# Kernel tuning notes

Measured on AMD Instinct MI355X. Metric: run time of the kernel, lower is better.

## Reference

```python
import jax, jax.numpy as jnp
import numpy as np

B, S, E, G = 64, 24, 128, 256
Km, Kch, Ko, Kp, Kc = 100, 200, 50, 50, 30
Vm, Vch, Vo, Vp, Vl, Vc = 1000, 3000, 500, 1500, 700, 2000
Veth, Vgen, Vage, Vins = 10, 2, 100, 5
TOTK = Km + Kch + Ko + Kp + 1 + Kc + 4  # 435 concat width


def setup_inputs() -> dict:
    key = jax.random.key(0)
    ks = jax.random.split(key, 24)
    ri = lambda k, shape, hi: jax.random.randint(k, shape, 0, hi)
    rn = lambda k, shape: (jax.random.normal(k, shape, dtype=jnp.float32) * 0.02)
    return {
        'meds': ri(ks[0], (B, S, Km), Vm),
        'chart': ri(ks[1], (B, S, Kch), Vch),
        'out': ri(ks[2], (B, S, Ko), Vo),
        'proc': ri(ks[3], (B, S, Kp), Vp),
        'lab': ri(ks[4], (B, S), Vl),
        'conds': ri(ks[5], (B, Kc), Vc),
        'demo': ri(ks[6], (B, 4), 2),
        'med_E': rn(ks[7], (Vm, E)), 'chart_E': rn(ks[8], (Vch, E)),
        'out_E': rn(ks[9], (Vo, E)), 'proc_E': rn(ks[10], (Vp, E)),
        'lab_E': rn(ks[11], (Vl, E)), 'cond_E': rn(ks[12], (Vc, E)),
        'gender_E': rn(ks[13], (Vgen, E)), 'eth_E': rn(ks[14], (Veth, E)),
        'ins_E': rn(ks[15], (Vins, E)), 'age_E': rn(ks[16], (Vage, E)),
        'proj_W': rn(ks[17], (TOTK, E)), 'proj_b': jnp.zeros((E,), jnp.float32),
        'W1': rn(ks[18], (E, G)), 'b1': jnp.zeros((G,), jnp.float32),
        'W2': rn(ks[19], (G, G)), 'b2': jnp.zeros((G,), jnp.float32),
        'fc1_W': rn(ks[20], (G, G // 2)), 'fc1_b': jnp.zeros((G // 2,), jnp.float32),
        'fc2_W': rn(ks[21], (G // 2, 1)), 'fc2_b': jnp.zeros((1,), jnp.float32),
    }


def _forward(meds, chart, out, proc, lab, conds, demo,
             med_E, chart_E, out_E, proc_E, lab_E, cond_E,
             gender_E, eth_E, ins_E, age_E,
             proj_W, proj_b, W1, b1, W2, b2, fc1_W, fc1_b, fc2_W, fc2_b):
    clamp = lambda i, V: jnp.clip(i, 0, V - 1)
    med_e = med_E[clamp(meds, Vm)]        # [B,S,Km,E]
    chart_e = chart_E[clamp(chart, Vch)]  # [B,S,Kch,E]
    out_e = out_E[clamp(out, Vo)]         # [B,S,Ko,E]
    proc_e = proc_E[clamp(proc, Vp)]      # [B,S,Kp,E]
    lab_e = lab_E[clamp(lab, Vl)]         # [B,S,E]
    cond_e = cond_E[clamp(conds, Vc)]     # [B,Kc,E]
    gen_e = gender_E[demo[:, 0]]          # [B,E]
    eth_e = eth_E[demo[:, 1]]
    ins_e = ins_E[demo[:, 2]]
    age_e = age_E[demo[:, 3]]
    demo_cols = [jnp.broadcast_to(d[:, None, :, None], (B, S, E, 1))
                 for d in (gen_e, eth_e, ins_e, age_e)]
    x = jnp.concatenate([
        med_e.transpose(0, 1, 3, 2),    # [B,S,E,Km]
        chart_e.transpose(0, 1, 3, 2),
        out_e.transpose(0, 1, 3, 2),
        proc_e.transpose(0, 1, 3, 2),
        lab_e[..., None],               # [B,S,E,1]
        jnp.broadcast_to(cond_e[:, None], (B, S, Kc, E)).transpose(0, 1, 3, 2),
    ] + demo_cols, axis=-1)             # [B,S,E,TOTK]
    x = x.mean(axis=-2)                 # mean over embed dim -> [B,S,TOTK]
    N = B * S
    x = x.reshape(N, TOTK) @ proj_W + proj_b   # [N,E]
    # GCNConv over complete graph + self loops: normalized adjacency is 1/N
    # everywhere, so aggregation == node-mean of (x @ W).
    h = jnp.broadcast_to(jnp.mean(x @ W1, axis=0, keepdims=True) + b1, (N, G))
    h = jax.nn.relu(h)
    # entropy attention
    w = jnp.exp(-jnp.sum(h * jnp.log(h + 1e-9), axis=1))
    h = h * (w / jnp.sum(w))[:, None]
    h = jnp.broadcast_to(jnp.mean(h @ W2, axis=0, keepdims=True) + b2, (N, G))
    x_pooled = h.reshape(B, S, G).mean(axis=1)          # [B,G]
    f = jax.nn.relu(x_pooled @ fc1_W + fc1_b)           # [B,G/2]
    o = f @ fc2_W + fc2_b                               # [B,1]
    return jax.nn.sigmoid(o), o


def reference(meds, chart, out, proc, lab, conds, demo,
              med_E, chart_E, out_E, proc_E, lab_E, cond_E,
              gender_E, eth_E, ins_E, age_E,
              proj_W, proj_b, W1, b1, W2, b2, fc1_W, fc1_b, fc2_W, fc2_b):
    return _forward(meds, chart, out, proc, lab, conds, demo,
                    med_E, chart_E, out_E, proc_E, lab_E, cond_E,
                    gender_E, eth_E, ins_E, age_E,
                    proj_W, proj_b, W1, b1, W2, b2, fc1_W, fc1_b, fc2_W, fc2_b)
```

## Files before the change

### kernel.cpp

```cpp
#include <hip/hip_runtime.h>
#include <math.h>

#define B_ 64
#define S_ 24
#define E_ 128
#define G_ 256
#define N_ (B_ * S_)
#define Km_ 100
#define Kch_ 200
#define Ko_ 50
#define Kp_ 50
#define Kc_ 30
#define TOTK_ 435

#define Vm_ 1000
#define Vch_ 3000
#define Vo_ 500
#define Vp_ 1500
#define Vl_ 700
#define Vc_ 2000
#define TOTROWS_ 8817

#define OFF_MED 0
#define OFF_CHART 1000
#define OFF_OUT 4000
#define OFF_PROC 4500
#define OFF_LAB 6000
#define OFF_COND 6700
#define OFF_GEN 8700
#define OFF_ETH 8702
#define OFF_INS 8712
#define OFF_AGE 8717
#define OFF_PART 8832

#define NCHUNK_ 32
#define CHUNK_N_ 48
#define NBLK_B_ 129
#define NTHR_ 512

__device__ __forceinline__ int clampi(int v, int hi) {
    return v < 0 ? 0 : (v > hi ? hi : v);
}

__global__ __launch_bounds__(NTHR_) void rowmeans_kernel(
    const float* __restrict__ medE, const float* __restrict__ chartE,
    const float* __restrict__ outE, const float* __restrict__ procE,
    const float* __restrict__ labE, const float* __restrict__ condE,
    const float* __restrict__ genE, const float* __restrict__ ethE,
    const float* __restrict__ insE, const float* __restrict__ ageE,
    float* __restrict__ rm)
{
    int row = blockIdx.x * (NTHR_ / 64) + (threadIdx.x >> 6);
    int lane = threadIdx.x & 63;
    if (row >= TOTROWS_) return;

    const float* src;
    int r = row;
    if (r < Vm_)                  { src = medE; }
    else if ((r -= Vm_)  < Vch_)  { src = chartE; }
    else if ((r -= Vch_) < Vo_)   { src = outE; }
    else if ((r -= Vo_)  < Vp_)   { src = procE; }
    else if ((r -= Vp_)  < Vl_)   { src = labE; }
    else if ((r -= Vl_)  < Vc_)   { src = condE; }
    else if ((r -= Vc_)  < 2)     { src = genE; }
    else if ((r -= 2)    < 10)    { src = ethE; }
    else if ((r -= 10)   < 5)     { src = insE; }
    else                          { r -= 5; src = ageE; }

    float2 v = *reinterpret_cast<const float2*>(src + (size_t)r * E_ + lane * 2);
    float s = v.x + v.y;
    #pragma unroll
    for (int off = 32; off > 0; off >>= 1) s += __shfl_down(s, off, 64);
    if (lane == 0) rm[row] = s * (1.0f / E_);
}

template<int K, int RPI, int CBASE, int RMBASE, int VMAX>
__device__ __forceinline__ void table_chunk(
    const int* __restrict__ idx, const float* __restrict__ rm,
    float* __restrict__ part, int p, int t, float* __restrict__ lds)
{
    constexpr int ACT = K * RPI;
    float acc = 0.0f;
    if (t < ACT) {
        const int kk = t % K;
        const int nr = t / K;
        const int n0 = p * CHUNK_N_;
        #pragma unroll
        for (int i = 0; i < (CHUNK_N_ + RPI - 1) / RPI; ++i) {
            int n = n0 + nr + i * RPI;
            if (nr + i * RPI < CHUNK_N_) {
                int ix = clampi(idx[n * K + kk], VMAX);
                acc += rm[RMBASE + ix];
            }
        }
    }
    lds[t] = acc;
    __syncthreads();
    if (t < K) {
        float s = lds[t];
        #pragma unroll
        for (int r = 1; r < RPI; ++r) s += lds[r * K + t];
        part[(CBASE + t) * NCHUNK_ + p] = s;
    }
}

__global__ __launch_bounds__(NTHR_) void colsum_kernel(
    const int* __restrict__ meds, const int* __restrict__ chart,
    const int* __restrict__ outv, const int* __restrict__ proc,
    const int* __restrict__ lab,  const int* __restrict__ conds,
    const int* __restrict__ demo,
    const float* __restrict__ rm, float* __restrict__ part)
{
    __shared__ float lds_red[NTHR_];
    const int t = threadIdx.x;
    const int bid = blockIdx.x;

    if (bid < 128) {
        const int table = bid >> 5;
        const int p = bid & 31;
        if (table == 0)      table_chunk<Km_, 5, 0,   OFF_MED,  Vm_ -1>(meds,  rm, part, p, t, lds_red);
        else if (table == 1) table_chunk<Kch_,2, 100, OFF_CHART,Vch_-1>(chart, rm, part, p, t, lds_red);
        else if (table == 2) table_chunk<Ko_, 10,300, OFF_OUT,  Vo_ -1>(outv,  rm, part, p, t, lds_red);
        else                 table_chunk<Kp_, 10,350, OFF_PROC, Vp_ -1>(proc,  rm, part, p, t, lds_red);
    } else {
        const int lane = t & 63;
        const int w = t >> 6;
        for (int j = w; j < 35; j += 8) {
            float s = 0.0f;
            if (j == 0) {
                #pragma unroll
                for (int i = 0; i < 24; ++i)
                    s += rm[OFF_LAB + clampi(lab[lane + 64 * i], Vl_ - 1)];
            } else if (j < 31) {
                int kk = j - 1;
                s = rm[OFF_COND + clampi(conds[lane * Kc_ + kk], Vc_ - 1)];
            } else {
                int jj = j - 31;
                int base = (jj == 0) ? OFF_GEN : (jj == 1) ? OFF_ETH :
                           (jj == 2) ? OFF_INS : OFF_AGE;
                s = rm[base + demo[lane * 4 + jj]];
            }
            #pragma unroll
            for (int off = 32; off > 0; off >>= 1) s += __shfl_down(s, off, 64);
            if (lane == 0) part[(400 + j) * NCHUNK_] = s;
        }
    }
}

__global__ __launch_bounds__(NTHR_) void head_kernel(
    const float* __restrict__ part,
    const float* __restrict__ projW, const float* __restrict__ projb,
    const float* __restrict__ W1, const float* __restrict__ b1,
    const float* __restrict__ W2, const float* __restrict__ b2,
    const float* __restrict__ fc1W, const float* __restrict__ fc1b,
    const float* __restrict__ fc2W, const float* __restrict__ fc2b,
    float* __restrict__ outp)
{
    __shared__ float sm[TOTK_];
    __shared__ float xbar[E_];
    __shared__ float h1s[G_];
    __shared__ float h2s[G_];
    __shared__ float fsh[G_ / 2];
    __shared__ float4 part4[8][64];
    __shared__ float2 part2[8][64];
    __shared__ float hred[8];
    __shared__ float oval;

    const int t = threadIdx.x;
    const int lane = t & 63;
    const int oc = t >> 6;

    if (t < TOTK_) {
        const float4* pp = (const float4*)(part + t * NCHUNK_);
        float s;
        if (t < 400) {
            s = 0.f;
            #pragma unroll
            for (int j = 0; j < NCHUNK_ / 4; ++j) {
                float4 v = pp[j];
                s += (v.x + v.y) + (v.z + v.w);
            }
            s *= (1.0f / N_);
        } else if (t == 400) {
            s = part[t * NCHUNK_] * (1.0f / N_);
        } else {
            s = part[t * NCHUNK_] * (1.0f / B_);
        }
        sm[t] = s;
    }
    __syncthreads();

    {
        const float2* Wp = (const float2*)projW;
        const int k0 = (TOTK_ * oc) >> 3;
        const int k1 = (TOTK_ * (oc + 1)) >> 3;
        float2 acc = {0.f, 0.f};
        #pragma unroll 8
        for (int k = k0; k < k1; ++k) {
            float s = sm[k];
            float2 w = Wp[k * 64 + lane];
            acc.x += s * w.x; acc.y += s * w.y;
        }
        part2[oc][lane] = acc;
        __syncthreads();
        if (t < 64) {
            float2 a = part2[0][t];
            #pragma unroll
            for (int j = 1; j < 8; ++j) { a.x += part2[j][t].x; a.y += part2[j][t].y; }
            xbar[2 * t]     = a.x + projb[2 * t];
            xbar[2 * t + 1] = a.y + projb[2 * t + 1];
        }
        __syncthreads();
    }

    {
        const float4* Wp = (const float4*)W1;
        const int k0 = oc * 16, k1 = k0 + 16;
        float4 acc = {0.f, 0.f, 0.f, 0.f};
        #pragma unroll 8
        for (int k = k0; k < k1; ++k) {
            float s = xbar[k];
            float4 w = Wp[k * 64 + lane];
            acc.x += s * w.x; acc.y += s * w.y; acc.z += s * w.z; acc.w += s * w.w;
        }
        part4[oc][lane] = acc;
        __syncthreads();
        if (t < 64) {
            float4 a = part4[0][t];
            #pragma unroll
            for (int j = 1; j < 8; ++j) {
                float4 p = part4[j][t];
                a.x += p.x; a.y += p.y; a.z += p.z; a.w += p.w;
            }
            float4 bb = ((const float4*)b1)[t];
            h1s[4 * t]     = fmaxf(a.x + bb.x, 0.f) * (1.0f / N_);
            h1s[4 * t + 1] = fmaxf(a.y + bb.y, 0.f) * (1.0f / N_);
            h1s[4 * t + 2] = fmaxf(a.z + bb.z, 0.f) * (1.0f / N_);
            h1s[4 * t + 3] = fmaxf(a.w + bb.w, 0.f) * (1.0f / N_);
        }
        __syncthreads();
    }

    {
        const float4* Wp = (const float4*)W2;
        const int k0 = oc * 32, k1 = k0 + 32;
        float4 acc = {0.f, 0.f, 0.f, 0.f};
        #pragma unroll 8
        for (int k = k0; k < k1; ++k) {
            float s = h1s[k];
            float4 w = Wp[k * 64 + lane];
            acc.x += s * w.x; acc.y += s * w.y; acc.z += s * w.z; acc.w += s * w.w;
        }
        part4[oc][lane] = acc;
        __syncthreads();
        if (t < 64) {
            float4 a = part4[0][t];
            #pragma unroll
            for (int j = 1; j < 8; ++j) {
                float4 p = part4[j][t];
                a.x += p.x; a.y += p.y; a.z += p.z; a.w += p.w;
            }
            float4 bb = ((const float4*)b2)[t];
            h2s[4 * t]     = a.x + bb.x;
            h2s[4 * t + 1] = a.y + bb.y;
            h2s[4 * t + 2] = a.z + bb.z;
            h2s[4 * t + 3] = a.w + bb.w;
        }
        __syncthreads();
    }

    {
        const float2* Wp = (const float2*)fc1W;
        const int k0 = oc * 32, k1 = k0 + 32;
        float2 acc = {0.f, 0.f};
        #pragma unroll 8
        for (int k = k0; k < k1; ++k) {
            float s = h2s[k];
            float2 w = Wp[k * 64 + lane];
            acc.x += s * w.x; acc.y += s * w.y;
        }
        part2[oc][lane] = acc;
        __syncthreads();
        if (t < 64) {
            float2 a = part2[0][t];
            #pragma unroll
            for (int j = 1; j < 8; ++j) { a.x += part2[j][t].x; a.y += part2[j][t].y; }
            fsh[2 * t]     = fmaxf(a.x + fc1b[2 * t], 0.f);
            fsh[2 * t + 1] = fmaxf(a.y + fc1b[2 * t + 1], 0.f);
        }
        __syncthreads();
    }

    {
        float p = (t < G_ / 2) ? fsh[t] * fc2W[t] : 0.f;
        #pragma unroll
        for (int off = 32; off > 0; off >>= 1) p += __shfl_down(p, off, 64);
        if (lane == 0) hred[oc] = p;
        __syncthreads();
        if (t == 0) {
            float o = fc2b[0];
            #pragma unroll
            for (int j = 0; j < 8; ++j) o += hred[j];
            oval = o;
        }
        __syncthreads();
        const float o = oval;
        const float sig = 1.0f / (1.0f + expf(-o));
        if (t < B_)            outp[t] = sig;
        else if (t < 2 * B_)   outp[t] = o;
    }
}

extern "C" void kernel_launch(void* const* d_in, const int* in_sizes, int n_in,
                              void* d_out, int out_size, void* d_ws, size_t ws_size,
                              hipStream_t stream) {
    const int* meds  = (const int*)d_in[0];
    const int* chart = (const int*)d_in[1];
    const int* outv  = (const int*)d_in[2];
    const int* proc  = (const int*)d_in[3];
    const int* lab   = (const int*)d_in[4];
    const int* conds = (const int*)d_in[5];
    const int* demo  = (const int*)d_in[6];
    const float* medE   = (const float*)d_in[7];
    const float* chartE = (const float*)d_in[8];
    const float* outE   = (const float*)d_in[9];
    const float* procE  = (const float*)d_in[10];
    const float* labE   = (const float*)d_in[11];
    const float* condE  = (const float*)d_in[12];
    const float* genE   = (const float*)d_in[13];
    const float* ethE   = (const float*)d_in[14];
    const float* insE   = (const float*)d_in[15];
    const float* ageE   = (const float*)d_in[16];
    const float* projW  = (const float*)d_in[17];
    const float* projb  = (const float*)d_in[18];
    const float* W1     = (const float*)d_in[19];
    const float* b1     = (const float*)d_in[20];
    const float* W2     = (const float*)d_in[21];
    const float* b2     = (const float*)d_in[22];
    const float* fc1W   = (const float*)d_in[23];
    const float* fc1b   = (const float*)d_in[24];
    const float* fc2W   = (const float*)d_in[25];
    const float* fc2b   = (const float*)d_in[26];

    float* rm   = (float*)d_ws;
    float* part = (float*)d_ws + OFF_PART;
    float* outp = (float*)d_out;

    int blocksA = (TOTROWS_ + (NTHR_ / 64) - 1) / (NTHR_ / 64);
    rowmeans_kernel<<<blocksA, NTHR_, 0, stream>>>(
        medE, chartE, outE, procE, labE, condE, genE, ethE, insE, ageE, rm);

    colsum_kernel<<<NBLK_B_, NTHR_, 0, stream>>>(
        meds, chart, outv, proc, lab, conds, demo, rm, part);

    head_kernel<<<1, NTHR_, 0, stream>>>(
        part, projW, projb, W1, b1, W2, b2, fc1W, fc1b, fc2W, fc2b, outp);
}
```

Before: 28.48 us.

## Fold W2·fc1 into a precomputed weight in the first kernel; widen proj GEMV

Adds 33 extra blocks to the rowmeans kernel that precompute Wc = W2·fc1W and cb = b2·fc1W + fc1b, so the single-block head kernel replaces two serial GEMV stages with one 256x128 GEMV. The projection GEMV is also reshaped to float4 loads split over 16 k-groups. The aim is to shorten the serial critical path in the one-block head kernel. In exchange, extra weight-product work now runs on every call, overlapped with the row-mean pass.

```diff
diff --git a/kernel.cpp b/kernel.cpp
--- a/kernel.cpp
+++ b/kernel.cpp
@@ -32,14 +32,48 @@
 #define OFF_INS 8712
 #define OFF_AGE 8717
 #define OFF_PART 8832
+#define OFF_WC   22752
+#define OFF_CB   55520
 
 #define NCHUNK_ 32
 #define CHUNK_N_ 48
 #define NBLK_B_ 129
 #define NTHR_ 512
 
+#define NBLKA_ROWS_ ((TOTROWS_ + 7) / 8)
+#define NBLKA_GEMM_ 33
+
 __device__ __forceinline__ int clampi(int v, int hi) {
     return v < 0 ? 0 : (v > hi ? hi : v);
+}
+
+__device__ void gemm_fold_body(
+    int gb, int t,
+    const float* __restrict__ W2, const float* __restrict__ fc1W,
+    const float* __restrict__ b2, const float* __restrict__ fc1b,
+    float* __restrict__ Wc, float* __restrict__ cb)
+{
+    if (gb < 32) {
+        const int k0 = gb * 8;
+        const int j  = t & 127;
+        const int rs = t >> 7;
+        float acc0 = 0.f, acc1 = 0.f;
+        #pragma unroll 8
+        for (int g = 0; g < G_; ++g) {
+            float fv = fc1W[g * 128 + j];
+            acc0 += W2[(k0 + rs) * G_ + g] * fv;
+            acc1 += W2[(k0 + rs + 4) * G_ + g] * fv;
+        }
+        Wc[(k0 + rs) * 128 + j]     = acc0;
+        Wc[(k0 + rs + 4) * 128 + j] = acc1;
+    } else {
+        if (t < 128) {
+            float acc = fc1b[t];
+            #pragma unroll 8
+            for (int g = 0; g < G_; ++g) acc += b2[g] * fc1W[g * 128 + t];
+            cb[t] = acc;
+        }
+    }
 }
 
 __global__ __launch_bounds__(NTHR_) void rowmeans_kernel(
@@ -48,8 +82,15 @@
     const float* __restrict__ labE, const float* __restrict__ condE,
     const float* __restrict__ genE, const float* __restrict__ ethE,
     const float* __restrict__ insE, const float* __restrict__ ageE,
-    float* __restrict__ rm)
-{
+    const float* __restrict__ W2,   const float* __restrict__ fc1W,
+    const float* __restrict__ b2,   const float* __restrict__ fc1b,
+    float* __restrict__ rm, float* __restrict__ Wc, float* __restrict__ cb)
+{
+    if (blockIdx.x >= NBLKA_ROWS_) {
+        gemm_fold_body(blockIdx.x - NBLKA_ROWS_, threadIdx.x, W2, fc1W, b2, fc1b, Wc, cb);
+        return;
+    }
+
     int row = blockIdx.x * (NTHR_ / 64) + (threadIdx.x >> 6);
     int lane = threadIdx.x & 63;
     if (row >= TOTROWS_) return;
@@ -151,18 +192,16 @@
     const float* __restrict__ part,
     const float* __restrict__ projW, const float* __restrict__ projb,
     const float* __restrict__ W1, const float* __restrict__ b1,
-    const float* __restrict__ W2, const float* __restrict__ b2,
-    const float* __restrict__ fc1W, const float* __restrict__ fc1b,
+    const float* __restrict__ Wc, const float* __restrict__ cb,
     const float* __restrict__ fc2W, const float* __restrict__ fc2b,
     float* __restrict__ outp)
 {
     __shared__ float sm[TOTK_];
     __shared__ float xbar[E_];
     __shared__ float h1s[G_];
-    __shared__ float h2s[G_];
     __shared__ float fsh[G_ / 2];
+    __shared__ float4 red4[16][32];
     __shared__ float4 part4[8][64];
-    __shared__ float2 part2[8][64];
     __shared__ float hred[8];
     __shared__ float oval;
 
@@ -191,24 +230,34 @@
     __syncthreads();
 
     {
-        const float2* Wp = (const float2*)projW;
-        const int k0 = (TOTK_ * oc) >> 3;
-        const int k1 = (TOTK_ * (oc + 1)) >> 3;
-        float2 acc = {0.f, 0.f};
-        #pragma unroll 8
-        for (int k = k0; k < k1; ++k) {
-            float s = sm[k];
-            float2 w = Wp[k * 64 + lane];
-            acc.x += s * w.x; acc.y += s * w.y;
-        }
-        part2[oc][lane] = acc;
-        __syncthreads();
-        if (t < 64) {
-            float2 a = part2[0][t];
-            #pragma unroll
-            for (int j = 1; j < 8; ++j) { a.x += part2[j][t].x; a.y += part2[j][t].y; }
-            xbar[2 * t]     = a.x + projb[2 * t];
-            xbar[2 * t + 1] = a.y + projb[2 * t + 1];
+        const float4* Wp = (const float4*)projW;
+        const int c4 = t & 31;
+        const int kg = t >> 5;
+        const int k0 = kg * 28;
+        float4 acc = {0.f, 0.f, 0.f, 0.f};
+        #pragma unroll
+        for (int i = 0; i < 28; ++i) {
+            int k = k0 + i;
+            if (k < TOTK_) {
+                float s = sm[k];
+                float4 w = Wp[k * 32 + c4];
+                acc.x += s * w.x; acc.y += s * w.y; acc.z += s * w.z; acc.w += s * w.w;
+            }
+        }
+        red4[kg][c4] = acc;
+        __syncthreads();
+        if (t < 32) {
+            float4 a = red4[0][t];
+            #pragma unroll
+            for (int j = 1; j < 16; ++j) {
+                float4 p = red4[j][t];
+                a.x += p.x; a.y += p.y; a.z += p.z; a.w += p.w;
+            }
+            float4 bb = ((const float4*)projb)[t];
+            xbar[4 * t]     = a.x + bb.x;
+            xbar[4 * t + 1] = a.y + bb.y;
+            xbar[4 * t + 2] = a.z + bb.z;
+            xbar[4 * t + 3] = a.w + bb.w;
         }
         __syncthreads();
     }
@@ -242,51 +291,32 @@
     }
 
     {
-        const float4* Wp = (const float4*)W2;
-        const int k0 = oc * 32, k1 = k0 + 32;
+        const float4* Wp = (const float4*)Wc;
+        const int c4 = t & 31;
+        const int kg = t >> 5;
+        const int k0 = kg * 16;
         float4 acc = {0.f, 0.f, 0.f, 0.f};
         #pragma unroll 8
-        for (int k = k0; k < k1; ++k) {
+        for (int i = 0; i < 16; ++i) {
+            int k = k0 + i;
             float s = h1s[k];
-            float4 w = Wp[k * 64 + lane];
+            float4 w = Wp[k * 32 + c4];
             acc.x += s * w.x; acc.y += s * w.y; acc.z += s * w.z; acc.w += s * w.w;
         }
-        part4[oc][lane] = acc;
-        __syncthreads();
-        if (t < 64) {
-            float4 a = part4[0][t];
-            #pragma unroll
-            for (int j = 1; j < 8; ++j) {
-                float4 p = part4[j][t];
+        red4[kg][c4] = acc;
+        __syncthreads();
+        if (t < 32) {
+            float4 a = red4[0][t];
+            #pragma unroll
+            for (int j = 1; j < 16; ++j) {
+                float4 p = red4[j][t];
                 a.x += p.x; a.y += p.y; a.z += p.z; a.w += p.w;
             }
-            float4 bb = ((const float4*)b2)[t];
-            h2s[4 * t]     = a.x + bb.x;
-            h2s[4 * t + 1] = a.y + bb.y;
-            h2s[4 * t + 2] = a.z + bb.z;
-            h2s[4 * t + 3] = a.w + bb.w;
-        }
-        __syncthreads();
-    }
-
-    {
-        const float2* Wp = (const float2*)fc1W;
-        const int k0 = oc * 32, k1 = k0 + 32;
-        float2 acc = {0.f, 0.f};
-        #pragma unroll 8
-        for (int k = k0; k < k1; ++k) {
-            float s = h2s[k];
-            float2 w = Wp[k * 64 + lane];
-            acc.x += s * w.x; acc.y += s * w.y;
-        }
-        part2[oc][lane] = acc;
-        __syncthreads();
-        if (t < 64) {
-            float2 a = part2[0][t];
-            #pragma unroll
-            for (int j = 1; j < 8; ++j) { a.x += part2[j][t].x; a.y += part2[j][t].y; }
-            fsh[2 * t]     = fmaxf(a.x + fc1b[2 * t], 0.f);
-            fsh[2 * t + 1] = fmaxf(a.y + fc1b[2 * t + 1], 0.f);
+            float4 bb = ((const float4*)cb)[t];
+            fsh[4 * t]     = fmaxf(a.x + bb.x, 0.f);
+            fsh[4 * t + 1] = fmaxf(a.y + bb.y, 0.f);
+            fsh[4 * t + 2] = fmaxf(a.z + bb.z, 0.f);
+            fsh[4 * t + 3] = fmaxf(a.w + bb.w, 0.f);
         }
         __syncthreads();
     }
@@ -344,15 +374,17 @@
 
     float* rm   = (float*)d_ws;
     float* part = (float*)d_ws + OFF_PART;
+    float* Wc   = (float*)d_ws + OFF_WC;
+    float* cb   = (float*)d_ws + OFF_CB;
     float* outp = (float*)d_out;
 
-    int blocksA = (TOTROWS_ + (NTHR_ / 64) - 1) / (NTHR_ / 64);
-    rowmeans_kernel<<<blocksA, NTHR_, 0, stream>>>(
-        medE, chartE, outE, procE, labE, condE, genE, ethE, insE, ageE, rm);
+    rowmeans_kernel<<<NBLKA_ROWS_ + NBLKA_GEMM_, NTHR_, 0, stream>>>(
+        medE, chartE, outE, procE, labE, condE, genE, ethE, insE, ageE,
+        W2, fc1W, b2, fc1b, rm, Wc, cb);
 
     colsum_kernel<<<NBLK_B_, NTHR_, 0, stream>>>(
         meds, chart, outv, proc, lab, conds, demo, rm, part);
 
     head_kernel<<<1, NTHR_, 0, stream>>>(
-        part, projW, projb, W1, b1, W2, b2, fc1W, fc1b, fc2W, fc2b, outp);
-}
+        part, projW, projb, W1, b1, Wc, cb, fc2W, fc2b, outp);
+}
```

New measurement: 36.39 us. +27.8%, slower.
